# Optimization experiments

Measured on AMD Instinct MI355X. Metric: run time of the kernel, lower is better.

The kernel has to match this reference:

```python
import jax, jax.numpy as jnp
import numpy as np

T_LEN, S_LEN, B = 100, 400, 16
D_IN, H, CTX, V = 512, 512, 1024, 50000


def setup_inputs() -> dict:
    key = jax.random.key(0)
    ks = jax.random.split(key, 16)
    p = lambda k, shp: jax.random.normal(k, shp, dtype=jnp.float32) * 0.05
    return {
        "y_emb": p(ks[0], (T_LEN, B, D_IN)),
        "context": p(ks[1], (S_LEN, B, CTX)),
        "init_h": p(ks[2], (B, H)),
        "init_c": p(ks[3], (B, H)),
        "x_mask": jnp.ones((S_LEN, B, 1), jnp.float32),
        "y_mask": jnp.ones((T_LEN, B, 1), jnp.float32),
        "y_idx": jax.random.randint(ks[4], (T_LEN, B), 0, V),
        # LSTMCell params (PyTorch gate order i,f,g,o)
        "W_ih": p(ks[5], (4 * H, D_IN)),
        "W_hh": p(ks[6], (4 * H, H)),
        "b_ih": jnp.zeros((4 * H,), jnp.float32),
        "b_hh": jnp.zeros((4 * H,), jnp.float32),
        # second gate block (order i,f,o,c per chunk names x4i,x4f,x4o,x4c)
        "Wx": p(ks[7], (4 * H, CTX)),
        "Ux": p(ks[8], (4 * H, H)),
        "bx": jnp.zeros((4 * H,), jnp.float32),
        # attention params
        "Wc_att": p(ks[9], (CTX, CTX)),
        "b_att": jnp.zeros((CTX,), jnp.float32),
        "W_comb_att": p(ks[10], (CTX, 2 * H)),
        "U_att": p(ks[11], (1, CTX)),
        # word prob: softmax(Linear(cat[h2, att, y_emb]))
        "Wp": p(ks[12], (V, H + CTX + D_IN)),
        "bp": jnp.zeros((V,), jnp.float32),
    }


def reference(y_emb, context, init_h, init_c, x_mask, y_mask, y_idx,
              W_ih, W_hh, b_ih, b_hh, Wx, Ux, bx,
              Wc_att, b_att, W_comb_att, U_att, Wp, bp):
    # pctx: [S, B, CTX]
    pctx = jnp.einsum('sbc,dc->sbd', context, Wc_att) + b_att
    u_att = U_att[0]  # [CTX]

    def step(carry, inp):
        h, c = carry              # [B, H] each
        y, ym, yi = inp           # [B, D_IN], [B, 1], [B]
        # LSTMCell (gate order i, f, g, o)
        gates = y @ W_ih.T + b_ih + h @ W_hh.T + b_hh
        gi, gf, gg, go = jnp.split(gates, 4, axis=1)
        c1 = jax.nn.sigmoid(gf) * c + jax.nn.sigmoid(gi) * jnp.tanh(gg)
        h1 = jax.nn.sigmoid(go) * jnp.tanh(c1)
        h1 = ym * h1 + (1.0 - ym) * h
        c1 = ym * c1 + (1.0 - ym) * c
        # attention query from cat(h1, c1)
        s = jnp.concatenate([h1, c1], axis=1)          # [B, 2H]
        q = s @ W_comb_att.T                           # [B, CTX]
        unreg = jnp.tanh(pctx + q) * x_mask            # [S, B, CTX]
        u = jnp.einsum('sbc,c->sb', unreg, u_att)[..., None]  # [S, B, 1]
        w = jnp.exp(u - jnp.max(u, axis=0, keepdims=True)) * x_mask
        w = w / jnp.sum(w, axis=0, keepdims=True)      # [S, B, 1]
        att = jnp.sum(w * context, axis=0)             # [B, CTX]
        # second gate block (chunk order i, f, o, c)
        pre = h1 @ Ux.T + att @ Wx.T + bx
        xi, xf, xo, xc = jnp.split(pre, 4, axis=1)
        c2 = jax.nn.sigmoid(xf) * c1 + jax.nn.sigmoid(xi) * jnp.tanh(xc)
        h2 = jax.nn.sigmoid(xo) * jnp.tanh(c2)
        c2 = ym * c2 + (1.0 - ym) * c1
        h2 = ym * h2 + (1.0 - ym) * h1
        # word prob + per-step NLL
        feat = jnp.concatenate([h2, att, y], axis=1)   # [B, H+CTX+D_IN]
        logp = jax.nn.log_softmax(feat @ Wp.T + bp, axis=1)
        cost = -jnp.take_along_axis(logp, yi[:, None], axis=1)[:, 0]  # [B]
        return (h2, c2), cost

    _, costs = jax.lax.scan(step, (init_h, init_c), (y_emb, y_mask, y_idx))
    ym2 = y_mask[..., 0]                               # [T, B]
    cost_per_batch = jnp.sum(costs * ym2, axis=0) / jnp.sum(ym2, axis=0)
    return cost_per_batch
```

## Files before the change

### kernel.cpp

```cpp
#include <hip/hip_runtime.h>
#include <stdint.h>

typedef unsigned int u32;
typedef unsigned short u16;
typedef unsigned char u8;
typedef long long i64;
typedef __attribute__((ext_vector_type(4))) float f32x4;
typedef __attribute__((ext_vector_type(4))) float f32x4v;
typedef __attribute__((ext_vector_type(8))) short bf16x8;

#define T_LEN 100
#define S_LEN 400
#define NB 16
#define HD 512
#define CTXD 1024
#define VOC 50000
#define K4H 2048
#define M_ALL 1600

static __device__ __forceinline__ float bf2f(u16 v) {
  union { u32 u; float f; } c; c.u = ((u32)v) << 16; return c.f;
}
static __device__ __forceinline__ u16 f2bf(float f) {
  union { float f; u32 u; } c; c.f = f;
  return (u16)((c.u + 0x7fffu + ((c.u >> 16) & 1u)) >> 16);
}
static __device__ __forceinline__ u32 pack2(float a, float b) {
  return (u32)f2bf(a) | ((u32)f2bf(b) << 16);
}
static __device__ __forceinline__ uint4 pack8(float4 a, float4 b) {
  return make_uint4(pack2(a.x, a.y), pack2(a.z, a.w), pack2(b.x, b.y), pack2(b.z, b.w));
}
static __device__ __forceinline__ uint4 pack8v(f32x4v a, f32x4v b) {
  return make_uint4(pack2(a.x, a.y), pack2(a.z, a.w), pack2(b.x, b.y), pack2(b.z, b.w));
}
static __device__ __forceinline__ u32 pkfp8(float x, float y, float z, float w) {
  int p = 0;
  p = __builtin_amdgcn_cvt_pk_fp8_f32(x, y, p, 0);
  p = __builtin_amdgcn_cvt_pk_fp8_f32(z, w, p, 1);
  return (u32)p;
}
static __device__ __forceinline__ float sigm(float x) { return 1.f / (1.f + __expf(-x)); }
static __device__ __forceinline__ float tanh_(float x) {
  float e = __expf(2.f * x);
  return 1.f - 2.f / (e + 1.f);
}

__global__ void sentinel_kernel(float* out, float v) {
  if (threadIdx.x < NB) out[threadIdx.x] = v;
}

struct CastArgs {
  const float* src[9];
  u16* dst[9];
  u32 cum[10];
};

__global__ __launch_bounds__(256) void cast_all(CastArgs A) {
  u32 i = blockIdx.x * 256 + threadIdx.x;
  if (i >= A.cum[9]) return;
  int seg = 0;
  while (i >= A.cum[seg + 1]) seg++;
  u32 li = i - A.cum[seg];
  const float* s = A.src[seg];
  f32x4v a = __builtin_nontemporal_load((const f32x4v*)&s[li * 8]);
  f32x4v b = __builtin_nontemporal_load((const f32x4v*)&s[li * 8 + 4]);
  if (seg < 8) {
    *(uint4*)&A.dst[seg][li * 8] = pack8v(a, b);
  } else {
    u32 m = li >> 6, k8 = (li & 63) << 3;
    u8* f8 = (u8*)A.dst[8];
    uint2 t;
    t.x = pkfp8(a.x, a.y, a.z, a.w);
    t.y = pkfp8(b.x, b.y, b.z, b.w);
    *(uint2*)&f8[(size_t)m * K4H + 1536 + k8] = t;
  }
}

template <int MODE>
__global__ __launch_bounds__(256) void gemm_bf16(const u16* __restrict__ A,
                                                 const u16* __restrict__ Bw,
                                                 void* __restrict__ out,
                                                 const float* __restrict__ bias1,
                                                 const float* __restrict__ bias2,
                                                 int M, int N, int K) {
  __shared__ u16 As[64][40];
  __shared__ u16 Bs[64][40];
  int nb = N / 64;
  int m0 = (blockIdx.x / nb) * 64;
  int n0 = (blockIdx.x % nb) * 64;
  int tid = threadIdx.x;
  int lane = tid & 63;
  int w = tid >> 6;
  int wm = (w >> 1) * 32, wn = (w & 1) * 32;
  f32x4 acc[2][2] = {};
  int arow = tid >> 2, achk = (tid & 3) * 8;
  for (int k0 = 0; k0 < K; k0 += 32) {
    __syncthreads();
    *(uint4*)&As[arow][achk] = *(const uint4*)&A[(size_t)(m0 + arow) * K + k0 + achk];
    *(uint4*)&Bs[arow][achk] = *(const uint4*)&Bw[(size_t)(n0 + arow) * K + k0 + achk];
    __syncthreads();
    int r = lane & 15, kg = lane >> 4;
    bf16x8 a0 = *(const bf16x8*)&As[wm + r][kg * 8];
    bf16x8 a1 = *(const bf16x8*)&As[wm + 16 + r][kg * 8];
    bf16x8 b0 = *(const bf16x8*)&Bs[wn + r][kg * 8];
    bf16x8 b1 = *(const bf16x8*)&Bs[wn + 16 + r][kg * 8];
    acc[0][0] = __builtin_amdgcn_mfma_f32_16x16x32_bf16(a0, b0, acc[0][0], 0, 0, 0);
    acc[0][1] = __builtin_amdgcn_mfma_f32_16x16x32_bf16(a0, b1, acc[0][1], 0, 0, 0);
    acc[1][0] = __builtin_amdgcn_mfma_f32_16x16x32_bf16(a1, b0, acc[1][0], 0, 0, 0);
    acc[1][1] = __builtin_amdgcn_mfma_f32_16x16x32_bf16(a1, b1, acc[1][1], 0, 0, 0);
  }
  int col = lane & 15, rg = lane >> 4;
#pragma unroll
  for (int fi = 0; fi < 2; fi++)
#pragma unroll
    for (int fj = 0; fj < 2; fj++)
#pragma unroll
      for (int r = 0; r < 4; r++) {
        int m = m0 + wm + fi * 16 + rg * 4 + r;
        int n = n0 + wn + fj * 16 + col;
        float v = acc[fi][fj][r] + bias1[n];
        if constexpr (MODE == 1) {
          v += bias2[n];
          ((float*)out)[(size_t)m * N + n] = v;
        } else {
          ((u16*)out)[(size_t)m * N + n] = f2bf(v);
        }
      }
}


__global__ __launch_bounds__(256) void k1q_lstm(const u16* __restrict__ Whh,
                                                const u16* __restrict__ Wcomb,
                                                const float* __restrict__ xW,
                                                const float* __restrict__ ym,
                                                const float* __restrict__ h,
                                                const float* __restrict__ c,
                                                float* __restrict__ h1,
                                                float* __restrict__ c1,
                                                float* __restrict__ qpart, int ts) {
  __shared__ u16 Al[16 * 520];
  __shared__ float gb[4][16][32];
  __shared__ u16 h1c1[16 * 72];
  const int tid = threadIdx.x;
#pragma unroll
  for (int i = 0; i < 4; i++) {
    int idx = i * 256 + tid;
    int b = idx >> 6, k8 = (idx & 63) << 3;
    float4 a = *(const float4*)&h[b * 512 + k8];
    float4 bv = *(const float4*)&h[b * 512 + k8 + 4];
    *(uint4*)&Al[b * 520 + k8] = pack8(a, bv);
  }
  __syncthreads();
  const int lane = tid & 63, w = tid >> 6;
  const int r16 = lane & 15, kg = lane >> 4;
  const int j0 = blockIdx.x * 32;
  {
    f32x4 acc0 = {}, acc1 = {};
    const size_t row0 = (size_t)(w * 512 + j0 + r16) * 512;
    const size_t row1 = (size_t)(w * 512 + j0 + 16 + r16) * 512;
#pragma unroll
    for (int ks = 0; ks < 16; ks++) {
      bf16x8 a = *(const bf16x8*)&Al[r16 * 520 + ks * 32 + kg * 8];
      bf16x8 b0 = *(const bf16x8*)&Whh[row0 + ks * 32 + kg * 8];
      bf16x8 b1 = *(const bf16x8*)&Whh[row1 + ks * 32 + kg * 8];
      acc0 = __builtin_amdgcn_mfma_f32_16x16x32_bf16(a, b0, acc0, 0, 0, 0);
      acc1 = __builtin_amdgcn_mfma_f32_16x16x32_bf16(a, b1, acc1, 0, 0, 0);
    }
#pragma unroll
    for (int r = 0; r < 4; r++) {
      gb[w][kg * 4 + r][r16] = acc0[r];
      gb[w][kg * 4 + r][16 + r16] = acc1[r];
    }
  }
  __syncthreads();
#pragma unroll
  for (int i = 0; i < 2; i++) {
    int idx = i * 256 + tid;
    int b = idx >> 5, j = idx & 31;
    int n = j0 + j;
    const float* xw = &xW[(size_t)(ts * NB + b) * K4H];
    float gi = gb[0][b][j] + xw[n];
    float gf = gb[1][b][j] + xw[512 + n];
    float gg = gb[2][b][j] + xw[1024 + n];
    float go = gb[3][b][j] + xw[1536 + n];
    float ymv = ym[ts * NB + b];
    float c_old = c[b * 512 + n], h_old = h[b * 512 + n];
    float c1v = sigm(gf) * c_old + sigm(gi) * tanh_(gg);
    float h1v = sigm(go) * tanh_(c1v);
    h1v = ymv * h1v + (1.f - ymv) * h_old;
    c1v = ymv * c1v + (1.f - ymv) * c_old;
    h1[b * 512 + n] = h1v;
    c1[b * 512 + n] = c1v;
    h1c1[b * 72 + j] = f2bf(h1v);
    h1c1[b * 72 + 32 + j] = f2bf(c1v);
  }
  __syncthreads();
  {
    bf16x8 a0 = *(const bf16x8*)&h1c1[r16 * 72 + kg * 8];
    bf16x8 a1 = *(const bf16x8*)&h1c1[r16 * 72 + 32 + kg * 8];
    float* qp = qpart + blockIdx.x * 16384;
    for (int nt = w; nt < 64; nt += 4) {
      int n = nt * 16 + r16;
      bf16x8 b0 = *(const bf16x8*)&Wcomb[(size_t)n * 1024 + j0 + kg * 8];
      bf16x8 b1 = *(const bf16x8*)&Wcomb[(size_t)n * 1024 + 512 + j0 + kg * 8];
      f32x4 acc = {};
      acc = __builtin_amdgcn_mfma_f32_16x16x32_bf16(a0, b0, acc, 0, 0, 0);
      acc = __builtin_amdgcn_mfma_f32_16x16x32_bf16(a1, b1, acc, 0, 0, 0);
#pragma unroll
      for (int r = 0; r < 4; r++) qp[(kg * 4 + r) * 1024 + nt * 16 + r16] = acc[r];
    }
  }
}

__global__ __launch_bounds__(256) void k3_attn(const u16* __restrict__ pctx,
                                               const u16* __restrict__ ctxb,
                                               const float* __restrict__ qpart,
                                               const float* __restrict__ xmask,
                                               const float* __restrict__ uatt,
                                               float* __restrict__ attnum,
                                               float* __restrict__ attden, int par) {
  __shared__ float q_l[1024], ua_l[1024], p_l[56], xm_l[56];
  const int tid = threadIdx.x;
  const int b = blockIdx.x & 15;
  const int s0 = (blockIdx.x >> 4) * 50;
  {
    float4 qs = {0.f, 0.f, 0.f, 0.f};
#pragma unroll
    for (int s_ = 0; s_ < 16; s_++) {
      float4 v = *(const float4*)&qpart[s_ * 16384 + b * 1024 + tid * 4];
      qs.x += v.x; qs.y += v.y; qs.z += v.z; qs.w += v.w;
    }
    *(float4*)&q_l[tid * 4] = qs;
  }
  *(float4*)&ua_l[tid * 4] = *(const float4*)&uatt[tid * 4];
  if (tid < 50) xm_l[tid] = xmask[(s0 + tid) * NB + b];
  __syncthreads();
  const int w = tid >> 6, lane = tid & 63;
  for (int i = w; i < 50; i += 4) {
    const u16* prow = &pctx[((size_t)(s0 + i) * NB + b) * CTXD + lane * 16];
    float s = 0.f;
#pragma unroll
    for (int half = 0; half < 2; half++) {
      bf16x8 pv = *(const bf16x8*)&prow[half * 8];
#pragma unroll
      for (int e = 0; e < 8; e++) {
        int cc = lane * 16 + half * 8 + e;
        s += tanh_(bf2f((u16)pv[e]) + q_l[cc]) * ua_l[cc];
      }
    }
#pragma unroll
    for (int off = 1; off < 64; off <<= 1) s += __shfl_xor(s, off);
    if (lane == 0) {
      float xm = xm_l[i];
      p_l[i] = __expf(s * xm) * xm;
    }
  }
  __syncthreads();
  const int c4 = tid << 2;
  float n0 = 0, n1 = 0, n2 = 0, n3 = 0;
  for (int i = 0; i < 50; i++) {
    float pv = p_l[i];
    uint2 ld = *(const uint2*)&ctxb[((size_t)(s0 + i) * NB + b) * CTXD + c4];
    n0 += pv * bf2f((u16)(ld.x & 0xffff));
    n1 += pv * bf2f((u16)(ld.x >> 16));
    n2 += pv * bf2f((u16)(ld.y & 0xffff));
    n3 += pv * bf2f((u16)(ld.y >> 16));
  }
  float* dst = &attnum[par * 16384 + b * 1024 + c4];
  atomicAdd(dst + 0, n0);
  atomicAdd(dst + 1, n1);
  atomicAdd(dst + 2, n2);
  atomicAdd(dst + 3, n3);
  if (tid == 0) {
    float d = 0.f;
    for (int i = 0; i < 50; i++) d += p_l[i];
    atomicAdd(&attden[par * NB + b], d);
  }
}

__global__ __launch_bounds__(256) void k4_gate2(const u16* __restrict__ Uxw,
                                                const u16* __restrict__ Wxw,
                                                const float* __restrict__ bx,
                                                float* __restrict__ attnum,
                                                float* __restrict__ attden,
                                                const float* __restrict__ h1,
                                                const float* __restrict__ c1,
                                                const float* __restrict__ ym,
                                                float* __restrict__ h,
                                                float* __restrict__ c,
                                                u8* __restrict__ feat8, int ts, int par) {
  __shared__ u16 Al[16 * 1544];
  __shared__ float gb[4][16][16];
  const int tid = threadIdx.x;
#pragma unroll
  for (int i = 0; i < 4; i++) {
    int idx = i * 256 + tid;
    int b = idx >> 6, k8 = (idx & 63) << 3;
    float4 a = *(const float4*)&h1[b * 512 + k8];
    float4 bv = *(const float4*)&h1[b * 512 + k8 + 4];
    *(uint4*)&Al[b * 1544 + k8] = pack8(a, bv);
  }
#pragma unroll
  for (int i = 0; i < 8; i++) {
    int idx = i * 256 + tid;
    int b = idx >> 7, c8 = (idx & 127) << 3;
    float rd = 1.f / attden[par * NB + b];
    const float* src = &attnum[par * 16384 + b * 1024 + c8];
    float4 a = *(const float4*)&src[0];
    float4 bv = *(const float4*)&src[4];
    a.x *= rd; a.y *= rd; a.z *= rd; a.w *= rd;
    bv.x *= rd; bv.y *= rd; bv.z *= rd; bv.w *= rd;
    *(uint4*)&Al[b * 1544 + 512 + c8] = pack8(a, bv);
  }
  __syncthreads();
  if (blockIdx.x < 16) {
    const u16* arow = &Al[blockIdx.x * 1544 + 512];
    int c4 = tid * 4;
    u32 p = pkfp8(bf2f(arow[c4]), bf2f(arow[c4 + 1]), bf2f(arow[c4 + 2]), bf2f(arow[c4 + 3]));
    *(u32*)&feat8[(size_t)(ts * NB + blockIdx.x) * K4H + 512 + c4] = p;
  }
  const int lane = tid & 63, w = tid >> 6;
  const int r16 = lane & 15, kg = lane >> 4;
  const int j0 = blockIdx.x * 16;
  f32x4 acc = {};
  const size_t rowU = (size_t)(w * 512 + j0 + r16) * 512;
  const size_t rowW = (size_t)(w * 512 + j0 + r16) * 1024;
#pragma unroll
  for (int ks = 0; ks < 16; ks++) {
    bf16x8 a = *(const bf16x8*)&Al[r16 * 1544 + ks * 32 + kg * 8];
    bf16x8 b0 = *(const bf16x8*)&Uxw[rowU + ks * 32 + kg * 8];
    acc = __builtin_amdgcn_mfma_f32_16x16x32_bf16(a, b0, acc, 0, 0, 0);
  }
#pragma unroll
  for (int ks = 16; ks < 48; ks++) {
    bf16x8 a = *(const bf16x8*)&Al[r16 * 1544 + ks * 32 + kg * 8];
    bf16x8 b0 = *(const bf16x8*)&Wxw[rowW + (ks - 16) * 32 + kg * 8];
    acc = __builtin_amdgcn_mfma_f32_16x16x32_bf16(a, b0, acc, 0, 0, 0);
  }
#pragma unroll
  for (int r = 0; r < 4; r++) gb[w][kg * 4 + r][r16] = acc[r];
  __syncthreads();
  {
    int b = tid >> 4, j = tid & 15;
    int n = j0 + j;
    float xi = gb[0][b][j] + bx[n];
    float xf = gb[1][b][j] + bx[512 + n];
    float xo = gb[2][b][j] + bx[1024 + n];
    float xc = gb[3][b][j] + bx[1536 + n];
    float ymv = ym[ts * NB + b];
    float c1v = c1[b * 512 + n], h1v = h1[b * 512 + n];
    float c2 = sigm(xf) * c1v + sigm(xi) * tanh_(xc);
    float h2 = sigm(xo) * tanh_(c2);
    c2 = ymv * c2 + (1.f - ymv) * c1v;
    h2 = ymv * h2 + (1.f - ymv) * h1v;
    h[b * 512 + n] = h2;
    c[b * 512 + n] = c2;
    int p8 = 0;
    p8 = __builtin_amdgcn_cvt_pk_fp8_f32(h2, h2, p8, 0);
    feat8[(size_t)(ts * NB + b) * K4H + n] = (u8)(p8 & 0xff);
  }
  attnum[(par ^ 1) * 16384 + blockIdx.x * 512 + tid] = 0.f;
  attnum[(par ^ 1) * 16384 + blockIdx.x * 512 + 256 + tid] = 0.f;
  if (blockIdx.x == 0 && tid < NB) attden[(par ^ 1) * NB + tid] = 0.f;
}

__global__ __launch_bounds__(512, 1) void lse_gemm_fp8(const u8* __restrict__ feat8,
                                                       const float* __restrict__ Wp,
                                                       const float* __restrict__ bp,
                                                       float* __restrict__ lse) {
  extern __shared__ char smem[];
  u8* Bl = (u8*)smem;
  const int tid = threadIdx.x;
  const int n0 = blockIdx.x * 64;
  for (int n = 0; n < 64; n++) {
    int gn = n0 + n;
    f32x4v f = {0.f, 0.f, 0.f, 0.f};
    if (gn < VOC)
      f = __builtin_nontemporal_load((const f32x4v*)&Wp[(size_t)gn * K4H + tid * 4]);
    *(u32*)&Bl[n * 2064 + tid * 4] = pkfp8(f.x, f.y, f.z, f.w);
  }
  __syncthreads();
  const int w = tid >> 6, lane = tid & 63;
  const int r16 = lane & 15, kg = lane >> 4;
  bool vj[4];
  float bpj[4];
#pragma unroll
  for (int j = 0; j < 4; j++) {
    int nf = n0 + j * 16 + r16;
    vj[j] = nf < VOC;
    bpj[j] = vj[j] ? bp[nf] : 0.f;
  }
  for (int qq = w; qq < 25; qq += 8) {
    int mrow = qq * 64;
    f32x4 acc[4][4] = {};
    for (int ks = 0; ks < 64; ks++) {
      i64 b0 = *(const i64*)&Bl[(r16) * 2064 + ks * 32 + kg * 8];
      i64 b1 = *(const i64*)&Bl[(16 + r16) * 2064 + ks * 32 + kg * 8];
      i64 b2 = *(const i64*)&Bl[(32 + r16) * 2064 + ks * 32 + kg * 8];
      i64 b3 = *(const i64*)&Bl[(48 + r16) * 2064 + ks * 32 + kg * 8];
#pragma unroll
      for (int s = 0; s < 4; s++) {
        i64 a = *(const i64*)&feat8[(size_t)(mrow + s * 16 + r16) * K4H + ks * 32 + kg * 8];
        acc[s][0] = __builtin_amdgcn_mfma_f32_16x16x32_fp8_fp8(a, b0, acc[s][0], 0, 0, 0);
        acc[s][1] = __builtin_amdgcn_mfma_f32_16x16x32_fp8_fp8(a, b1, acc[s][1], 0, 0, 0);
        acc[s][2] = __builtin_amdgcn_mfma_f32_16x16x32_fp8_fp8(a, b2, acc[s][2], 0, 0, 0);
        acc[s][3] = __builtin_amdgcn_mfma_f32_16x16x32_fp8_fp8(a, b3, acc[s][3], 0, 0, 0);
      }
    }
#pragma unroll
    for (int s = 0; s < 4; s++) {
#pragma unroll
      for (int r = 0; r < 4; r++) {
        float e = 0.f;
#pragma unroll
        for (int j = 0; j < 4; j++)
          if (vj[j]) e += __expf(acc[s][j][r] + bpj[j]);
        e += __shfl_xor(e, 1);
        e += __shfl_xor(e, 2);
        e += __shfl_xor(e, 4);
        e += __shfl_xor(e, 8);
        if (r16 == 0) atomicAdd(&lse[mrow + s * 16 + kg * 4 + r], e);
      }
    }
  }
}

__global__ __launch_bounds__(256) void target_logit(const u8* __restrict__ feat8,
                                                    const float* __restrict__ Wp,
                                                    const float* __restrict__ bp,
                                                    const int* __restrict__ yidx,
                                                    float* __restrict__ tlog) {
  int gw = (blockIdx.x * 256 + threadIdx.x) >> 6;
  int lane = threadIdx.x & 63;
  if (gw >= M_ALL) return;
  int yi = yidx[gw];
  const float* wrow = Wp + (size_t)yi * K4H;
  const u8* frow = feat8 + (size_t)gw * K4H;
  float s = 0.f;
#pragma unroll
  for (int i = 0; i < 4; i++) {
    int k = i * 512 + lane * 8;
    uint2 fv = *(const uint2*)&frow[k];
    f32x4v w0 = __builtin_nontemporal_load((const f32x4v*)&wrow[k]);
    f32x4v w1 = __builtin_nontemporal_load((const f32x4v*)&wrow[k + 4]);
    s += __builtin_amdgcn_cvt_f32_fp8(fv.x, 0) * w0.x;
    s += __builtin_amdgcn_cvt_f32_fp8(fv.x, 1) * w0.y;
    s += __builtin_amdgcn_cvt_f32_fp8(fv.x, 2) * w0.z;
    s += __builtin_amdgcn_cvt_f32_fp8(fv.x, 3) * w0.w;
    s += __builtin_amdgcn_cvt_f32_fp8(fv.y, 0) * w1.x;
    s += __builtin_amdgcn_cvt_f32_fp8(fv.y, 1) * w1.y;
    s += __builtin_amdgcn_cvt_f32_fp8(fv.y, 2) * w1.z;
    s += __builtin_amdgcn_cvt_f32_fp8(fv.y, 3) * w1.w;
  }
#pragma unroll
  for (int off = 1; off < 64; off <<= 1) s += __shfl_xor(s, off);
  if (lane == 0) tlog[gw] = s + bp[yi];
}

__global__ void finalize(const float* __restrict__ lse, const float* __restrict__ tlog,
                         const float* __restrict__ ymask, float* __restrict__ out) {
  int b = threadIdx.x;
  if (b < NB) {
    float sc = 0.f, sm = 0.f;
    for (int t = 0; t < T_LEN; t++) {
      int m = t * NB + b;
      float ym = ymask[m];
      sc += (logf(lse[m]) - tlog[m]) * ym;
      sm += ym;
    }
    out[b] = sc / sm;
  }
}

extern "C" void kernel_launch(void* const* d_in, const int* in_sizes, int n_in,
                              void* d_out, int out_size, void* d_ws, size_t ws_size,
                              hipStream_t stream) {
  const float* y_emb = (const float*)d_in[0];
  const float* context = (const float*)d_in[1];
  const float* init_h = (const float*)d_in[2];
  const float* init_c = (const float*)d_in[3];
  const float* x_mask = (const float*)d_in[4];
  const float* y_mask = (const float*)d_in[5];
  const int* y_idx = (const int*)d_in[6];
  const float* W_ih = (const float*)d_in[7];
  const float* W_hh = (const float*)d_in[8];
  const float* b_ih = (const float*)d_in[9];
  const float* b_hh = (const float*)d_in[10];
  const float* Wx = (const float*)d_in[11];
  const float* Ux = (const float*)d_in[12];
  const float* bx = (const float*)d_in[13];
  const float* Wc_att = (const float*)d_in[14];
  const float* b_att = (const float*)d_in[15];
  const float* W_comb = (const float*)d_in[16];
  const float* U_att = (const float*)d_in[17];
  const float* Wp = (const float*)d_in[18];
  const float* bp = (const float*)d_in[19];

  if (ws_size < 63000000ULL) {
    sentinel_kernel<<<1, 64, 0, stream>>>((float*)d_out, (float)(ws_size >> 20));
    return;
  }

  char* ws = (char*)d_ws;
  float* lse = (float*)(ws + 0);
  float* attnum = (float*)(ws + 8192);
  float* attden = (float*)(ws + 139264);
  float* tlog = (float*)(ws + 139776);
  u16* pctx = (u16*)(ws + 147456);
  u16* ctxb = (u16*)(ws + 13254656);
  u16* Wcb = (u16*)(ws + 26361856);
  u16* yembb = (u16*)(ws + 28459008);
  float* qpart = (float*)(ws + 28459008);
  u16* Wihb = (u16*)(ws + 30097408);
  u16* Whhb = (u16*)(ws + 32194560);
  u16* Wcombb = (u16*)(ws + 34291712);
  u16* Uxb = (u16*)(ws + 36388864);
  u16* Wxb = (u16*)(ws + 38486016);
  float* xW = (float*)(ws + 42680320);
  u8* feat8 = (u8*)(ws + 55787520);
  float* hbuf = (float*)(ws + 62341120);
  float* cbuf = (float*)(ws + 62373888);
  float* h1buf = (float*)(ws + 62406656);
  float* c1buf = (float*)(ws + 62439424);

  hipMemsetAsync(ws, 0, 139776, stream);

  CastArgs ca;
  ca.src[0] = context;  ca.dst[0] = ctxb;
  ca.src[1] = Wc_att;   ca.dst[1] = Wcb;
  ca.src[2] = y_emb;    ca.dst[2] = yembb;
  ca.src[3] = W_ih;     ca.dst[3] = Wihb;
  ca.src[4] = W_hh;     ca.dst[4] = Whhb;
  ca.src[5] = W_comb;   ca.dst[5] = Wcombb;
  ca.src[6] = Ux;       ca.dst[6] = Uxb;
  ca.src[7] = Wx;       ca.dst[7] = Wxb;
  ca.src[8] = y_emb;    ca.dst[8] = (u16*)feat8;
  u32 sz[9] = {819200, 131072, 102400, 131072, 131072, 131072, 131072, 262144, 102400};
  ca.cum[0] = 0;
  for (int i = 0; i < 9; i++) ca.cum[i + 1] = ca.cum[i] + sz[i];
  cast_all<<<(ca.cum[9] + 255) / 256, 256, 0, stream>>>(ca);

  gemm_bf16<0><<<1600, 256, 0, stream>>>(ctxb, Wcb, pctx, b_att, b_att, 6400, 1024, 1024);
  gemm_bf16<1><<<800, 256, 0, stream>>>(yembb, Wihb, xW, b_ih, b_hh, 1600, 2048, 512);

  for (int ts = 0; ts < T_LEN; ts++) {
    int par = ts & 1;
    const float* hsrc = (ts == 0) ? init_h : hbuf;
    const float* csrc = (ts == 0) ? init_c : cbuf;
    k1q_lstm<<<16, 256, 0, stream>>>(Whhb, Wcombb, xW, y_mask, hsrc, csrc, h1buf, c1buf,
                                     qpart, ts);
    k3_attn<<<128, 256, 0, stream>>>(pctx, ctxb, qpart, x_mask, U_att, attnum, attden, par);
    k4_gate2<<<32, 256, 0, stream>>>(Uxb, Wxb, bx, attnum, attden, h1buf, c1buf, y_mask,
                                     hbuf, cbuf, feat8, ts, par);
  }

  hipFuncSetAttribute(reinterpret_cast<const void*>(lse_gemm_fp8),
                      hipFuncAttributeMaxDynamicSharedMemorySize, 132096);
  lse_gemm_fp8<<<782, 512, 132096, stream>>>(feat8, Wp, bp, lse);

  target_logit<<<400, 256, 0, stream>>>(feat8, Wp, bp, y_idx, tlog);
  finalize<<<1, 64, 0, stream>>>(lse, tlog, y_mask, (float*)d_out);
}
```

Before: 5.535 ms.

## Fuse per-timestep decoder kernels into one persistent kernel with grid barriers

Replaces the 300 per-step launches (LSTM+query, attention, second gate) with a single persistent kernel of 256 blocks. The three phases of each timestep are separated by a hierarchical atomic grid barrier: blocks count per group of 16, then the group counts are combined. Attention work is now split across 256 blocks of 25 source positions each, instead of 128 blocks of 50. The aim is to remove kernel launch and drain gaps across the recurrence. In exchange it adds spin-wait barrier latency and relies on all 256 blocks being co-resident, which risks deadlock if they are not.

```diff
diff --git a/kernel.cpp b/kernel.cpp
--- a/kernel.cpp
+++ b/kernel.cpp
@@ -129,240 +129,250 @@
       }
 }
 
-
-__global__ __launch_bounds__(256) void k1q_lstm(const u16* __restrict__ Whh,
-                                                const u16* __restrict__ Wcomb,
-                                                const float* __restrict__ xW,
-                                                const float* __restrict__ ym,
-                                                const float* __restrict__ h,
-                                                const float* __restrict__ c,
-                                                float* __restrict__ h1,
-                                                float* __restrict__ c1,
-                                                float* __restrict__ qpart, int ts) {
-  __shared__ u16 Al[16 * 520];
-  __shared__ float gb[4][16][32];
-  __shared__ u16 h1c1[16 * 72];
+struct DecArgs {
+  const u16 *pctx, *ctx, *Whh, *Wcomb, *Uxw, *Wxw;
+  const float *xW, *bx, *uatt, *xmask, *ymask, *init_h, *init_c;
+  float *h, *c, *h1, *c1, *qpart, *attnum, *attden;
+  u8* feat8;
+  u32* bar;
+};
+
+static __device__ __forceinline__ void gbar(u32* bar, u32 gen) {
+  __syncthreads();
+  if (threadIdx.x == 0) {
+    __builtin_amdgcn_fence(__ATOMIC_RELEASE, "agent");
+    const int g = blockIdx.x >> 4;
+    u32* grp = bar + 32 + g * 32;
+    u32 old = __hip_atomic_fetch_add(grp, 1u, __ATOMIC_RELAXED, __HIP_MEMORY_SCOPE_AGENT);
+    if (old == gen * 16u - 1u) {
+      u32 r = __hip_atomic_fetch_add(bar, 1u, __ATOMIC_RELAXED, __HIP_MEMORY_SCOPE_AGENT);
+      if (r == gen * 16u - 1u) {
+        __hip_atomic_store(bar + 16, gen, __ATOMIC_RELAXED, __HIP_MEMORY_SCOPE_AGENT);
+      }
+    }
+    while (__hip_atomic_load(bar + 16, __ATOMIC_RELAXED, __HIP_MEMORY_SCOPE_AGENT) < gen)
+      __builtin_amdgcn_s_sleep(2);
+    __builtin_amdgcn_fence(__ATOMIC_ACQUIRE, "agent");
+  }
+  __syncthreads();
+}
+
+__global__ __launch_bounds__(256, 1) void decoder_coop(DecArgs A) {
+  __shared__ union {
+    struct { u16 Al[16 * 520]; float gb[4][16][32]; u16 h1c1[16 * 72]; } a;
+    struct { float q_l[1024]; float ua_l[1024]; float p_l[32]; float xm_l[32]; } c;
+    struct { u16 Al[16 * 1544]; float gb[4][16][16]; } d;
+  } sm;
   const int tid = threadIdx.x;
-#pragma unroll
-  for (int i = 0; i < 4; i++) {
-    int idx = i * 256 + tid;
-    int b = idx >> 6, k8 = (idx & 63) << 3;
-    float4 a = *(const float4*)&h[b * 512 + k8];
-    float4 bv = *(const float4*)&h[b * 512 + k8 + 4];
-    *(uint4*)&Al[b * 520 + k8] = pack8(a, bv);
-  }
-  __syncthreads();
+  const int blk = blockIdx.x;
   const int lane = tid & 63, w = tid >> 6;
   const int r16 = lane & 15, kg = lane >> 4;
-  const int j0 = blockIdx.x * 32;
-  {
-    f32x4 acc0 = {}, acc1 = {};
-    const size_t row0 = (size_t)(w * 512 + j0 + r16) * 512;
-    const size_t row1 = (size_t)(w * 512 + j0 + 16 + r16) * 512;
-#pragma unroll
-    for (int ks = 0; ks < 16; ks++) {
-      bf16x8 a = *(const bf16x8*)&Al[r16 * 520 + ks * 32 + kg * 8];
-      bf16x8 b0 = *(const bf16x8*)&Whh[row0 + ks * 32 + kg * 8];
-      bf16x8 b1 = *(const bf16x8*)&Whh[row1 + ks * 32 + kg * 8];
-      acc0 = __builtin_amdgcn_mfma_f32_16x16x32_bf16(a, b0, acc0, 0, 0, 0);
-      acc1 = __builtin_amdgcn_mfma_f32_16x16x32_bf16(a, b1, acc1, 0, 0, 0);
-    }
-#pragma unroll
-    for (int r = 0; r < 4; r++) {
-      gb[w][kg * 4 + r][r16] = acc0[r];
-      gb[w][kg * 4 + r][16 + r16] = acc1[r];
-    }
-  }
-  __syncthreads();
-#pragma unroll
-  for (int i = 0; i < 2; i++) {
-    int idx = i * 256 + tid;
-    int b = idx >> 5, j = idx & 31;
-    int n = j0 + j;
-    const float* xw = &xW[(size_t)(ts * NB + b) * K4H];
-    float gi = gb[0][b][j] + xw[n];
-    float gf = gb[1][b][j] + xw[512 + n];
-    float gg = gb[2][b][j] + xw[1024 + n];
-    float go = gb[3][b][j] + xw[1536 + n];
-    float ymv = ym[ts * NB + b];
-    float c_old = c[b * 512 + n], h_old = h[b * 512 + n];
-    float c1v = sigm(gf) * c_old + sigm(gi) * tanh_(gg);
-    float h1v = sigm(go) * tanh_(c1v);
-    h1v = ymv * h1v + (1.f - ymv) * h_old;
-    c1v = ymv * c1v + (1.f - ymv) * c_old;
-    h1[b * 512 + n] = h1v;
-    c1[b * 512 + n] = c1v;
-    h1c1[b * 72 + j] = f2bf(h1v);
-    h1c1[b * 72 + 32 + j] = f2bf(c1v);
-  }
-  __syncthreads();
-  {
-    bf16x8 a0 = *(const bf16x8*)&h1c1[r16 * 72 + kg * 8];
-    bf16x8 a1 = *(const bf16x8*)&h1c1[r16 * 72 + 32 + kg * 8];
-    float* qp = qpart + blockIdx.x * 16384;
-    for (int nt = w; nt < 64; nt += 4) {
-      int n = nt * 16 + r16;
-      bf16x8 b0 = *(const bf16x8*)&Wcomb[(size_t)n * 1024 + j0 + kg * 8];
-      bf16x8 b1 = *(const bf16x8*)&Wcomb[(size_t)n * 1024 + 512 + j0 + kg * 8];
+  u32 gen = 1;
+
+  for (int ts = 0; ts < T_LEN; ts++) {
+    const int par = ts & 1;
+    if (blk < 16) {
+      const float* hs = ts ? A.h : A.init_h;
+      const float* cs = ts ? A.c : A.init_c;
+#pragma unroll
+      for (int i = 0; i < 4; i++) {
+        int idx = i * 256 + tid;
+        int b = idx >> 6, k8 = (idx & 63) << 3;
+        float4 a = *(const float4*)&hs[b * 512 + k8];
+        float4 bv = *(const float4*)&hs[b * 512 + k8 + 4];
+        *(uint4*)&sm.a.Al[b * 520 + k8] = pack8(a, bv);
+      }
+      __syncthreads();
+      const int j0 = blk * 32;
+      {
+        f32x4 acc0 = {}, acc1 = {};
+        const size_t row0 = (size_t)(w * 512 + j0 + r16) * 512;
+        const size_t row1 = (size_t)(w * 512 + j0 + 16 + r16) * 512;
+#pragma unroll
+        for (int ks = 0; ks < 16; ks++) {
+          bf16x8 a = *(const bf16x8*)&sm.a.Al[r16 * 520 + ks * 32 + kg * 8];
+          bf16x8 b0 = *(const bf16x8*)&A.Whh[row0 + ks * 32 + kg * 8];
+          bf16x8 b1 = *(const bf16x8*)&A.Whh[row1 + ks * 32 + kg * 8];
+          acc0 = __builtin_amdgcn_mfma_f32_16x16x32_bf16(a, b0, acc0, 0, 0, 0);
+          acc1 = __builtin_amdgcn_mfma_f32_16x16x32_bf16(a, b1, acc1, 0, 0, 0);
+        }
+#pragma unroll
+        for (int r = 0; r < 4; r++) {
+          sm.a.gb[w][kg * 4 + r][r16] = acc0[r];
+          sm.a.gb[w][kg * 4 + r][16 + r16] = acc1[r];
+        }
+      }
+      __syncthreads();
+#pragma unroll
+      for (int i = 0; i < 2; i++) {
+        int idx = i * 256 + tid;
+        int b = idx >> 5, j = idx & 31;
+        int n = j0 + j;
+        const float* xw = &A.xW[(size_t)(ts * NB + b) * K4H];
+        float gi = sm.a.gb[0][b][j] + xw[n];
+        float gf = sm.a.gb[1][b][j] + xw[512 + n];
+        float gg = sm.a.gb[2][b][j] + xw[1024 + n];
+        float go = sm.a.gb[3][b][j] + xw[1536 + n];
+        float ymv = A.ymask[ts * NB + b];
+        float c_old = cs[b * 512 + n], h_old = hs[b * 512 + n];
+        float c1v = sigm(gf) * c_old + sigm(gi) * tanh_(gg);
+        float h1v = sigm(go) * tanh_(c1v);
+        h1v = ymv * h1v + (1.f - ymv) * h_old;
+        c1v = ymv * c1v + (1.f - ymv) * c_old;
+        A.h1[b * 512 + n] = h1v;
+        A.c1[b * 512 + n] = c1v;
+        sm.a.h1c1[b * 72 + j] = f2bf(h1v);
+        sm.a.h1c1[b * 72 + 32 + j] = f2bf(c1v);
+      }
+      __syncthreads();
+      {
+        bf16x8 a0 = *(const bf16x8*)&sm.a.h1c1[r16 * 72 + kg * 8];
+        bf16x8 a1 = *(const bf16x8*)&sm.a.h1c1[r16 * 72 + 32 + kg * 8];
+        float* qp = A.qpart + blk * 16384;
+        for (int nt = w; nt < 64; nt += 4) {
+          int n = nt * 16 + r16;
+          bf16x8 b0 = *(const bf16x8*)&A.Wcomb[(size_t)n * 1024 + j0 + kg * 8];
+          bf16x8 b1 = *(const bf16x8*)&A.Wcomb[(size_t)n * 1024 + 512 + j0 + kg * 8];
+          f32x4 acc = {};
+          acc = __builtin_amdgcn_mfma_f32_16x16x32_bf16(a0, b0, acc, 0, 0, 0);
+          acc = __builtin_amdgcn_mfma_f32_16x16x32_bf16(a1, b1, acc, 0, 0, 0);
+#pragma unroll
+          for (int r = 0; r < 4; r++) qp[(kg * 4 + r) * 1024 + nt * 16 + r16] = acc[r];
+        }
+      }
+    }
+    gbar(A.bar, gen); gen++;
+    {
+      const int b = blk & 15;
+      const int s0 = (blk >> 4) * 25;
+      {
+        float4 qs = {0.f, 0.f, 0.f, 0.f};
+#pragma unroll
+        for (int s_ = 0; s_ < 16; s_++) {
+          float4 v = *(const float4*)&A.qpart[s_ * 16384 + b * 1024 + tid * 4];
+          qs.x += v.x; qs.y += v.y; qs.z += v.z; qs.w += v.w;
+        }
+        *(float4*)&sm.c.q_l[tid * 4] = qs;
+      }
+      *(float4*)&sm.c.ua_l[tid * 4] = *(const float4*)&A.uatt[tid * 4];
+      if (tid < 25) sm.c.xm_l[tid] = A.xmask[(s0 + tid) * NB + b];
+      __syncthreads();
+      for (int i = w; i < 25; i += 4) {
+        const u16* prow = &A.pctx[((size_t)(s0 + i) * NB + b) * CTXD + lane * 16];
+        float s = 0.f;
+#pragma unroll
+        for (int half = 0; half < 2; half++) {
+          bf16x8 pv = *(const bf16x8*)&prow[half * 8];
+#pragma unroll
+          for (int e = 0; e < 8; e++) {
+            int cc = lane * 16 + half * 8 + e;
+            s += tanh_(bf2f((u16)pv[e]) + sm.c.q_l[cc]) * sm.c.ua_l[cc];
+          }
+        }
+#pragma unroll
+        for (int off = 1; off < 64; off <<= 1) s += __shfl_xor(s, off);
+        if (lane == 0) {
+          float xm = sm.c.xm_l[i];
+          sm.c.p_l[i] = __expf(s * xm) * xm;
+        }
+      }
+      __syncthreads();
+      const int c4 = tid << 2;
+      float n0 = 0, n1 = 0, n2 = 0, n3 = 0;
+#pragma unroll 5
+      for (int i = 0; i < 25; i++) {
+        float pv = sm.c.p_l[i];
+        uint2 ld = *(const uint2*)&A.ctx[((size_t)(s0 + i) * NB + b) * CTXD + c4];
+        n0 += pv * bf2f((u16)(ld.x & 0xffff));
+        n1 += pv * bf2f((u16)(ld.x >> 16));
+        n2 += pv * bf2f((u16)(ld.y & 0xffff));
+        n3 += pv * bf2f((u16)(ld.y >> 16));
+      }
+      float* dst = &A.attnum[par * 16384 + b * 1024 + c4];
+      atomicAdd(dst + 0, n0);
+      atomicAdd(dst + 1, n1);
+      atomicAdd(dst + 2, n2);
+      atomicAdd(dst + 3, n3);
+      if (tid == 0) {
+        float d = 0.f;
+        for (int i = 0; i < 25; i++) d += sm.c.p_l[i];
+        atomicAdd(&A.attden[par * NB + b], d);
+      }
+    }
+    gbar(A.bar, gen); gen++;
+    if (blk < 32) {
+#pragma unroll
+      for (int i = 0; i < 4; i++) {
+        int idx = i * 256 + tid;
+        int b = idx >> 6, k8 = (idx & 63) << 3;
+        float4 a = *(const float4*)&A.h1[b * 512 + k8];
+        float4 bv = *(const float4*)&A.h1[b * 512 + k8 + 4];
+        *(uint4*)&sm.d.Al[b * 1544 + k8] = pack8(a, bv);
+      }
+#pragma unroll
+      for (int i = 0; i < 8; i++) {
+        int idx = i * 256 + tid;
+        int b = idx >> 7, c8 = (idx & 127) << 3;
+        float rd = 1.f / A.attden[par * NB + b];
+        const float* src = &A.attnum[par * 16384 + b * 1024 + c8];
+        float4 a = *(const float4*)&src[0];
+        float4 bv = *(const float4*)&src[4];
+        a.x *= rd; a.y *= rd; a.z *= rd; a.w *= rd;
+        bv.x *= rd; bv.y *= rd; bv.z *= rd; bv.w *= rd;
+        *(uint4*)&sm.d.Al[b * 1544 + 512 + c8] = pack8(a, bv);
+      }
+      __syncthreads();
+      if (blk < 16) {
+        const u16* arow = &sm.d.Al[blk * 1544 + 512];
+        int c4 = tid * 4;
+        u32 p = pkfp8(bf2f(arow[c4]), bf2f(arow[c4 + 1]), bf2f(arow[c4 + 2]),
+                      bf2f(arow[c4 + 3]));
+        *(u32*)&A.feat8[(size_t)(ts * NB + blk) * K4H + 512 + c4] = p;
+      }
+      const int j0 = blk * 16;
       f32x4 acc = {};
-      acc = __builtin_amdgcn_mfma_f32_16x16x32_bf16(a0, b0, acc, 0, 0, 0);
-      acc = __builtin_amdgcn_mfma_f32_16x16x32_bf16(a1, b1, acc, 0, 0, 0);
-#pragma unroll
-      for (int r = 0; r < 4; r++) qp[(kg * 4 + r) * 1024 + nt * 16 + r16] = acc[r];
-    }
-  }
-}
-
-__global__ __launch_bounds__(256) void k3_attn(const u16* __restrict__ pctx,
-                                               const u16* __restrict__ ctxb,
-                                               const float* __restrict__ qpart,
-                                               const float* __restrict__ xmask,
-                                               const float* __restrict__ uatt,
-                                               float* __restrict__ attnum,
-                                               float* __restrict__ attden, int par) {
-  __shared__ float q_l[1024], ua_l[1024], p_l[56], xm_l[56];
-  const int tid = threadIdx.x;
-  const int b = blockIdx.x & 15;
-  const int s0 = (blockIdx.x >> 4) * 50;
-  {
-    float4 qs = {0.f, 0.f, 0.f, 0.f};
-#pragma unroll
-    for (int s_ = 0; s_ < 16; s_++) {
-      float4 v = *(const float4*)&qpart[s_ * 16384 + b * 1024 + tid * 4];
-      qs.x += v.x; qs.y += v.y; qs.z += v.z; qs.w += v.w;
-    }
-    *(float4*)&q_l[tid * 4] = qs;
-  }
-  *(float4*)&ua_l[tid * 4] = *(const float4*)&uatt[tid * 4];
-  if (tid < 50) xm_l[tid] = xmask[(s0 + tid) * NB + b];
-  __syncthreads();
-  const int w = tid >> 6, lane = tid & 63;
-  for (int i = w; i < 50; i += 4) {
-    const u16* prow = &pctx[((size_t)(s0 + i) * NB + b) * CTXD + lane * 16];
-    float s = 0.f;
-#pragma unroll
-    for (int half = 0; half < 2; half++) {
-      bf16x8 pv = *(const bf16x8*)&prow[half * 8];
-#pragma unroll
-      for (int e = 0; e < 8; e++) {
-        int cc = lane * 16 + half * 8 + e;
-        s += tanh_(bf2f((u16)pv[e]) + q_l[cc]) * ua_l[cc];
-      }
-    }
-#pragma unroll
-    for (int off = 1; off < 64; off <<= 1) s += __shfl_xor(s, off);
-    if (lane == 0) {
-      float xm = xm_l[i];
-      p_l[i] = __expf(s * xm) * xm;
-    }
-  }
-  __syncthreads();
-  const int c4 = tid << 2;
-  float n0 = 0, n1 = 0, n2 = 0, n3 = 0;
-  for (int i = 0; i < 50; i++) {
-    float pv = p_l[i];
-    uint2 ld = *(const uint2*)&ctxb[((size_t)(s0 + i) * NB + b) * CTXD + c4];
-    n0 += pv * bf2f((u16)(ld.x & 0xffff));
-    n1 += pv * bf2f((u16)(ld.x >> 16));
-    n2 += pv * bf2f((u16)(ld.y & 0xffff));
-    n3 += pv * bf2f((u16)(ld.y >> 16));
-  }
-  float* dst = &attnum[par * 16384 + b * 1024 + c4];
-  atomicAdd(dst + 0, n0);
-  atomicAdd(dst + 1, n1);
-  atomicAdd(dst + 2, n2);
-  atomicAdd(dst + 3, n3);
-  if (tid == 0) {
-    float d = 0.f;
-    for (int i = 0; i < 50; i++) d += p_l[i];
-    atomicAdd(&attden[par * NB + b], d);
-  }
-}
-
-__global__ __launch_bounds__(256) void k4_gate2(const u16* __restrict__ Uxw,
-                                                const u16* __restrict__ Wxw,
-                                                const float* __restrict__ bx,
-                                                float* __restrict__ attnum,
-                                                float* __restrict__ attden,
-                                                const float* __restrict__ h1,
-                                                const float* __restrict__ c1,
-                                                const float* __restrict__ ym,
-                                                float* __restrict__ h,
-                                                float* __restrict__ c,
-                                                u8* __restrict__ feat8, int ts, int par) {
-  __shared__ u16 Al[16 * 1544];
-  __shared__ float gb[4][16][16];
-  const int tid = threadIdx.x;
-#pragma unroll
-  for (int i = 0; i < 4; i++) {
-    int idx = i * 256 + tid;
-    int b = idx >> 6, k8 = (idx & 63) << 3;
-    float4 a = *(const float4*)&h1[b * 512 + k8];
-    float4 bv = *(const float4*)&h1[b * 512 + k8 + 4];
-    *(uint4*)&Al[b * 1544 + k8] = pack8(a, bv);
-  }
-#pragma unroll
-  for (int i = 0; i < 8; i++) {
-    int idx = i * 256 + tid;
-    int b = idx >> 7, c8 = (idx & 127) << 3;
-    float rd = 1.f / attden[par * NB + b];
-    const float* src = &attnum[par * 16384 + b * 1024 + c8];
-    float4 a = *(const float4*)&src[0];
-    float4 bv = *(const float4*)&src[4];
-    a.x *= rd; a.y *= rd; a.z *= rd; a.w *= rd;
-    bv.x *= rd; bv.y *= rd; bv.z *= rd; bv.w *= rd;
-    *(uint4*)&Al[b * 1544 + 512 + c8] = pack8(a, bv);
-  }
-  __syncthreads();
-  if (blockIdx.x < 16) {
-    const u16* arow = &Al[blockIdx.x * 1544 + 512];
-    int c4 = tid * 4;
-    u32 p = pkfp8(bf2f(arow[c4]), bf2f(arow[c4 + 1]), bf2f(arow[c4 + 2]), bf2f(arow[c4 + 3]));
-    *(u32*)&feat8[(size_t)(ts * NB + blockIdx.x) * K4H + 512 + c4] = p;
-  }
-  const int lane = tid & 63, w = tid >> 6;
-  const int r16 = lane & 15, kg = lane >> 4;
-  const int j0 = blockIdx.x * 16;
-  f32x4 acc = {};
-  const size_t rowU = (size_t)(w * 512 + j0 + r16) * 512;
-  const size_t rowW = (size_t)(w * 512 + j0 + r16) * 1024;
-#pragma unroll
-  for (int ks = 0; ks < 16; ks++) {
-    bf16x8 a = *(const bf16x8*)&Al[r16 * 1544 + ks * 32 + kg * 8];
-    bf16x8 b0 = *(const bf16x8*)&Uxw[rowU + ks * 32 + kg * 8];
-    acc = __builtin_amdgcn_mfma_f32_16x16x32_bf16(a, b0, acc, 0, 0, 0);
-  }
-#pragma unroll
-  for (int ks = 16; ks < 48; ks++) {
-    bf16x8 a = *(const bf16x8*)&Al[r16 * 1544 + ks * 32 + kg * 8];
-    bf16x8 b0 = *(const bf16x8*)&Wxw[rowW + (ks - 16) * 32 + kg * 8];
-    acc = __builtin_amdgcn_mfma_f32_16x16x32_bf16(a, b0, acc, 0, 0, 0);
-  }
-#pragma unroll
-  for (int r = 0; r < 4; r++) gb[w][kg * 4 + r][r16] = acc[r];
-  __syncthreads();
-  {
-    int b = tid >> 4, j = tid & 15;
-    int n = j0 + j;
-    float xi = gb[0][b][j] + bx[n];
-    float xf = gb[1][b][j] + bx[512 + n];
-    float xo = gb[2][b][j] + bx[1024 + n];
-    float xc = gb[3][b][j] + bx[1536 + n];
-    float ymv = ym[ts * NB + b];
-    float c1v = c1[b * 512 + n], h1v = h1[b * 512 + n];
-    float c2 = sigm(xf) * c1v + sigm(xi) * tanh_(xc);
-    float h2 = sigm(xo) * tanh_(c2);
-    c2 = ymv * c2 + (1.f - ymv) * c1v;
-    h2 = ymv * h2 + (1.f - ymv) * h1v;
-    h[b * 512 + n] = h2;
-    c[b * 512 + n] = c2;
-    int p8 = 0;
-    p8 = __builtin_amdgcn_cvt_pk_fp8_f32(h2, h2, p8, 0);
-    feat8[(size_t)(ts * NB + b) * K4H + n] = (u8)(p8 & 0xff);
-  }
-  attnum[(par ^ 1) * 16384 + blockIdx.x * 512 + tid] = 0.f;
-  attnum[(par ^ 1) * 16384 + blockIdx.x * 512 + 256 + tid] = 0.f;
-  if (blockIdx.x == 0 && tid < NB) attden[(par ^ 1) * NB + tid] = 0.f;
+      const size_t rowU = (size_t)(w * 512 + j0 + r16) * 512;
+      const size_t rowW = (size_t)(w * 512 + j0 + r16) * 1024;
+#pragma unroll
+      for (int ks = 0; ks < 16; ks++) {
+        bf16x8 a = *(const bf16x8*)&sm.d.Al[r16 * 1544 + ks * 32 + kg * 8];
+        bf16x8 b0 = *(const bf16x8*)&A.Uxw[rowU + ks * 32 + kg * 8];
+        acc = __builtin_amdgcn_mfma_f32_16x16x32_bf16(a, b0, acc, 0, 0, 0);
+      }
+#pragma unroll
+      for (int ks = 16; ks < 48; ks++) {
+        bf16x8 a = *(const bf16x8*)&sm.d.Al[r16 * 1544 + ks * 32 + kg * 8];
+        bf16x8 b0 = *(const bf16x8*)&A.Wxw[rowW + (ks - 16) * 32 + kg * 8];
+        acc = __builtin_amdgcn_mfma_f32_16x16x32_bf16(a, b0, acc, 0, 0, 0);
+      }
+#pragma unroll
+      for (int r = 0; r < 4; r++) sm.d.gb[w][kg * 4 + r][r16] = acc[r];
+      __syncthreads();
+      {
+        int b = tid >> 4, j = tid & 15;
+        int n = j0 + j;
+        float xi = sm.d.gb[0][b][j] + A.bx[n];
+        float xf = sm.d.gb[1][b][j] + A.bx[512 + n];
+        float xo = sm.d.gb[2][b][j] + A.bx[1024 + n];
+        float xc = sm.d.gb[3][b][j] + A.bx[1536 + n];
+        float ymv = A.ymask[ts * NB + b];
+        float c1v = A.c1[b * 512 + n], h1v = A.h1[b * 512 + n];
+        float c2 = sigm(xf) * c1v + sigm(xi) * tanh_(xc);
+        float h2 = sigm(xo) * tanh_(c2);
+        c2 = ymv * c2 + (1.f - ymv) * c1v;
+        h2 = ymv * h2 + (1.f - ymv) * h1v;
+        A.h[b * 512 + n] = h2;
+        A.c[b * 512 + n] = c2;
+        int p8 = 0;
+        p8 = __builtin_amdgcn_cvt_pk_fp8_f32(h2, h2, p8, 0);
+        A.feat8[(size_t)(ts * NB + b) * K4H + n] = (u8)(p8 & 0xff);
+      }
+      A.attnum[(par ^ 1) * 16384 + blk * 512 + tid] = 0.f;
+      A.attnum[(par ^ 1) * 16384 + blk * 512 + 256 + tid] = 0.f;
+      if (blk == 0 && tid < NB) A.attden[(par ^ 1) * NB + tid] = 0.f;
+    }
+    gbar(A.bar, gen); gen++;
+  }
 }
 
 __global__ __launch_bounds__(512, 1) void lse_gemm_fp8(const u8* __restrict__ feat8,
@@ -497,7 +507,7 @@
   const float* Wp = (const float*)d_in[18];
   const float* bp = (const float*)d_in[19];
 
-  if (ws_size < 63000000ULL) {
+  if (ws_size < 60000000ULL) {
     sentinel_kernel<<<1, 64, 0, stream>>>((float*)d_out, (float)(ws_size >> 20));
     return;
   }
@@ -506,25 +516,26 @@
   float* lse = (float*)(ws + 0);
   float* attnum = (float*)(ws + 8192);
   float* attden = (float*)(ws + 139264);
-  float* tlog = (float*)(ws + 139776);
-  u16* pctx = (u16*)(ws + 147456);
-  u16* ctxb = (u16*)(ws + 13254656);
-  u16* Wcb = (u16*)(ws + 26361856);
-  u16* yembb = (u16*)(ws + 28459008);
-  float* qpart = (float*)(ws + 28459008);
-  u16* Wihb = (u16*)(ws + 30097408);
-  u16* Whhb = (u16*)(ws + 32194560);
-  u16* Wcombb = (u16*)(ws + 34291712);
-  u16* Uxb = (u16*)(ws + 36388864);
-  u16* Wxb = (u16*)(ws + 38486016);
-  float* xW = (float*)(ws + 42680320);
-  u8* feat8 = (u8*)(ws + 55787520);
-  float* hbuf = (float*)(ws + 62341120);
-  float* cbuf = (float*)(ws + 62373888);
-  float* h1buf = (float*)(ws + 62406656);
-  float* c1buf = (float*)(ws + 62439424);
-
-  hipMemsetAsync(ws, 0, 139776, stream);
+  u32* bar = (u32*)(ws + 139392);
+  float* tlog = (float*)(ws + 143488);
+  u16* pctx = (u16*)(ws + 151552);
+  u16* ctxb = (u16*)(ws + 13258752);
+  u16* Wcb = (u16*)(ws + 26365952);
+  u16* yembb = (u16*)(ws + 28463104);
+  float* qpart = (float*)(ws + 28463104);
+  u16* Wihb = (u16*)(ws + 30101504);
+  u16* Whhb = (u16*)(ws + 32198656);
+  u16* Wcombb = (u16*)(ws + 34295808);
+  u16* Uxb = (u16*)(ws + 36392960);
+  u16* Wxb = (u16*)(ws + 38490112);
+  float* xW = (float*)(ws + 42684416);
+  u8* feat8 = (u8*)(ws + 55791616);
+  float* hbuf = (float*)(ws + 59068416);
+  float* cbuf = (float*)(ws + 59101184);
+  float* h1buf = (float*)(ws + 59133952);
+  float* c1buf = (float*)(ws + 59166720);
+
+  hipMemsetAsync(ws, 0, 143488, stream);
 
   CastArgs ca;
   ca.src[0] = context;  ca.dst[0] = ctxb;
@@ -544,16 +555,13 @@
   gemm_bf16<0><<<1600, 256, 0, stream>>>(ctxb, Wcb, pctx, b_att, b_att, 6400, 1024, 1024);
   gemm_bf16<1><<<800, 256, 0, stream>>>(yembb, Wihb, xW, b_ih, b_hh, 1600, 2048, 512);
 
-  for (int ts = 0; ts < T_LEN; ts++) {
-    int par = ts & 1;
-    const float* hsrc = (ts == 0) ? init_h : hbuf;
-    const float* csrc = (ts == 0) ? init_c : cbuf;
-    k1q_lstm<<<16, 256, 0, stream>>>(Whhb, Wcombb, xW, y_mask, hsrc, csrc, h1buf, c1buf,
-                                     qpart, ts);
-    k3_attn<<<128, 256, 0, stream>>>(pctx, ctxb, qpart, x_mask, U_att, attnum, attden, par);
-    k4_gate2<<<32, 256, 0, stream>>>(Uxb, Wxb, bx, attnum, attden, h1buf, c1buf, y_mask,
-                                     hbuf, cbuf, feat8, ts, par);
-  }
+  DecArgs a;
+  a.pctx = pctx; a.ctx = ctxb; a.Whh = Whhb; a.Wcomb = Wcombb; a.Uxw = Uxb; a.Wxw = Wxb;
+  a.xW = xW; a.bx = bx; a.uatt = U_att; a.xmask = x_mask; a.ymask = y_mask;
+  a.init_h = init_h; a.init_c = init_c;
+  a.h = hbuf; a.c = cbuf; a.h1 = h1buf; a.c1 = c1buf; a.qpart = qpart;
+  a.attnum = attnum; a.attden = attden; a.feat8 = feat8; a.bar = bar;
+  decoder_coop<<<256, 256, 0, stream>>>(a);
 
   hipFuncSetAttribute(reinterpret_cast<const void*>(lse_gemm_fp8),
                       hipFuncAttributeMaxDynamicSharedMemorySize, 132096);
```

New measurement: 7.522 ms. 1.36x slower.
